# Optimization experiments

Hardware: AMD Instinct MI355X
Metric: run time of the kernel (lower is better)

Reference implementation:

```python
import jax, jax.numpy as jnp
import numpy as np

B, S, D = 2, 2048, 1024
H, DK, DV = 16, 64, 64
EPS = 1e-5
SQRT_DK = float(np.sqrt(DK))


def setup_inputs() -> dict:
    key = jax.random.key(0)
    ks = jax.random.split(key, 8)
    sc = 0.02
    return {
        "x": jax.random.normal(ks[0], (B, S, D), jnp.float32),
        "Wk": jax.random.normal(ks[1], (D, H * DK), jnp.float32) * sc,
        "bk": jnp.zeros((H * DK,), jnp.float32),
        "Wq": jax.random.normal(ks[2], (D, H * DK), jnp.float32) * sc,
        "bq": jnp.zeros((H * DK,), jnp.float32),
        "Wv": jax.random.normal(ks[3], (D, H * DV), jnp.float32) * sc,
        "bv": jnp.zeros((H * DV,), jnp.float32),
        "Wo": jax.random.normal(ks[4], (H * DV, D), jnp.float32) * sc,
        "bo": jnp.zeros((D,), jnp.float32),
        "gamma": jnp.ones((D,), jnp.float32),
        "beta": jnp.zeros((D,), jnp.float32),
    }


def reference(x, Wk, bk, Wq, bq, Wv, bv, Wo, bo, gamma, beta):
    b, s, d = x.shape
    # NOTE: original torch code reshapes (B, S, H*dk) directly to (B, H, S, dk)
    # without a transpose; we replicate that exact (non-standard) reshape.
    keys = (x @ Wk + bk).reshape(b, H, s, DK)
    queries = (x @ Wq + bq).reshape(b, H, s, DK)
    values = (x @ Wv + bv).reshape(b, H, s, DV)

    scores = jnp.einsum('bhqd,bhkd->bhqk', queries, keys) / SQRT_DK
    causal_mask = jnp.triu(jnp.ones((s, s), bool), k=1)  # True = masked
    scores = jnp.where(causal_mask[None, None], jnp.float32(-1e9), scores)
    attention = jax.nn.softmax(scores, axis=-1)

    context = jnp.einsum('bhqk,bhkd->bhqd', attention, values)
    context = context.reshape(b, s, H * DV)

    out = context @ Wo + bo  # dropout is identity at inference
    out = out + x            # residual connection

    mean = jnp.mean(out, axis=-1, keepdims=True)
    var = jnp.mean(jnp.square(out - mean), axis=-1, keepdims=True)
    return (out - mean) / jnp.sqrt(var + EPS) * gamma + beta
```

## Files before the change

### kernel.cpp

```cpp
#include <hip/hip_runtime.h>


typedef __attribute__((ext_vector_type(8))) __bf16 bf16x8;
typedef __attribute__((ext_vector_type(8))) unsigned short ushort8;
typedef __attribute__((ext_vector_type(4))) unsigned short u16x4;
typedef __attribute__((ext_vector_type(4))) float f32x4;

static __device__ __forceinline__ unsigned short f2bf(float f) {
    unsigned u = __builtin_bit_cast(unsigned, f);
    u += 0x7fffu + ((u >> 16) & 1u);
    return (unsigned short)(u >> 16);
}

static __device__ __forceinline__ float bf2f(unsigned short u) {
    return __builtin_bit_cast(float, (unsigned)u << 16);
}

__global__ __launch_bounds__(256) void prep_kernel(
    const float* __restrict__ x,
    const float* __restrict__ Wq, const float* __restrict__ Wk,
    const float* __restrict__ Wv, const float* __restrict__ Wo,
    unsigned short* __restrict__ xb, unsigned short* __restrict__ WT)
{
    const int tid = threadIdx.x;
    const int z = blockIdx.z;
    if (z == 4) {
        const int bid = blockIdx.y * 16 + blockIdx.x;
        const int base = bid * 4096 + tid;
        #pragma unroll
        for (int it = 0; it < 16; it++) {
            int i = base + it * 256;
            float4 v = ((const float4*)x)[i];
            ushort4 o;
            o.x = f2bf(v.x); o.y = f2bf(v.y); o.z = f2bf(v.z); o.w = f2bf(v.w);
            ((ushort4*)xb)[i] = o;
        }
        return;
    }
    const float* src = (z == 0) ? Wq : (z == 1) ? Wk : (z == 2) ? Wv : Wo;
    unsigned short* dst = WT + ((size_t)z << 20);
    __shared__ __align__(16) unsigned short t[64 * 68];
    const int n0 = blockIdx.x * 64, k0 = blockIdx.y * 64;
    #pragma unroll
    for (int u = 0; u < 4; u++) {
        int e = u * 256 + tid;
        int r = e >> 4, c4 = (e & 15) * 4;
        float4 v = *(const float4*)(src + (k0 + r) * 1024 + n0 + c4);
        ushort4 o;
        o.x = f2bf(v.x); o.y = f2bf(v.y); o.z = f2bf(v.z); o.w = f2bf(v.w);
        *(ushort4*)(t + r * 68 + c4) = o;
    }
    __syncthreads();
    #pragma unroll
    for (int u = 0; u < 4; u++) {
        int e = u * 256 + tid;
        int rn = e >> 4, ck = (e & 15) * 4;
        ushort4 o;
        o.x = t[(ck + 0) * 68 + rn];
        o.y = t[(ck + 1) * 68 + rn];
        o.z = t[(ck + 2) * 68 + rn];
        o.w = t[(ck + 3) * 68 + rn];
        *(ushort4*)(dst + (n0 + rn) * 1024 + k0 + ck) = o;
    }
}

__global__ __launch_bounds__(256) void vtrans_kernel(const unsigned short* __restrict__ V,
                                                     unsigned short* __restrict__ VT) {
    __shared__ __align__(16) unsigned short t[64 * 68];
    const int tid = threadIdx.x;
    const int p0 = blockIdx.x * 64;
    const long base = (long)blockIdx.y * 131072;
    #pragma unroll
    for (int u = 0; u < 2; u++) {
        int e = u * 256 + tid;
        int r = e >> 3, c8 = (e & 7) * 8;
        ushort8 v = *(const ushort8*)(V + base + (long)(p0 + r) * 64 + c8);
        *(ushort8*)(t + r * 68 + c8) = v;
    }
    __syncthreads();
    #pragma unroll
    for (int u = 0; u < 4; u++) {
        int e = u * 256 + tid;
        int dv = e >> 4, pk = (e & 15) * 4;
        ushort4 o;
        o.x = t[(pk + 0) * 68 + dv];
        o.y = t[(pk + 1) * 68 + dv];
        o.z = t[(pk + 2) * 68 + dv];
        o.w = t[(pk + 3) * 68 + dv];
        *(ushort4*)(VT + base + (long)dv * 2048 + p0 + pk) = o;
    }
}

__global__ __launch_bounds__(256, 3) void gemm_kernel(
    const unsigned short* __restrict__ A,
    const unsigned short* __restrict__ Bt,
    const float* __restrict__ b0, const float* __restrict__ b1, const float* __restrict__ b2,
    unsigned short* __restrict__ outQ, unsigned short* __restrict__ outK,
    unsigned short* __restrict__ outV,
    const float* __restrict__ resid, int mode)
{
    __shared__ __align__(16) unsigned short As[2][128 * 32];
    __shared__ __align__(16) unsigned short Bs[2][128 * 32];
    const int tid = threadIdx.x;
    const int lane = tid & 63, wave = tid >> 6;
    const int quad = lane >> 4, l16 = lane & 15;
    const int wm = wave >> 1, wn = wave & 1;
    const int row0 = blockIdx.y * 128, n0g = blockIdx.x * 128;

    const int sr = tid >> 2;
    const int sc = (tid & 3) * 8;
    const unsigned short* Ag0 = A + (size_t)(row0 + sr) * 1024 + sc;
    const unsigned short* Ag1 = A + (size_t)(row0 + 64 + sr) * 1024 + sc;
    const unsigned short* Bg0 = Bt + (size_t)(n0g + sr) * 1024 + sc;
    const unsigned short* Bg1 = Bt + (size_t)(n0g + 64 + sr) * 1024 + sc;

    {
        ushort8 a0 = *(const ushort8*)(Ag0);
        ushort8 a1 = *(const ushort8*)(Ag1);
        ushort8 bv0 = *(const ushort8*)(Bg0);
        ushort8 bv1 = *(const ushort8*)(Bg1);
        *(ushort8*)(As[0] + sr * 32 + sc) = a0;
        *(ushort8*)(As[0] + (64 + sr) * 32 + sc) = a1;
        *(ushort8*)(Bs[0] + sr * 32 + sc) = bv0;
        *(ushort8*)(Bs[0] + (64 + sr) * 32 + sc) = bv1;
    }
    __syncthreads();

    f32x4 acc[4][4] = {};
    #pragma unroll 2
    for (int it = 0; it < 32; ++it) {
        const int cur = it & 1;
        ushort8 na0, na1, nb0, nb1;
        if (it < 31) {
            const int k0 = (it + 1) * 32;
            na0 = *(const ushort8*)(Ag0 + k0);
            na1 = *(const ushort8*)(Ag1 + k0);
            nb0 = *(const ushort8*)(Bg0 + k0);
            nb1 = *(const ushort8*)(Bg1 + k0);
        }
        bf16x8 af[4], bfr[4];
        #pragma unroll
        for (int i = 0; i < 4; i++)
            af[i] = *(const bf16x8*)(As[cur] + (wm * 64 + i * 16 + l16) * 32 + quad * 8);
        #pragma unroll
        for (int j = 0; j < 4; j++)
            bfr[j] = *(const bf16x8*)(Bs[cur] + (wn * 64 + j * 16 + l16) * 32 + quad * 8);
        #pragma unroll
        for (int i = 0; i < 4; i++)
            #pragma unroll
            for (int j = 0; j < 4; j++)
                acc[i][j] = __builtin_amdgcn_mfma_f32_16x16x32_bf16(af[i], bfr[j], acc[i][j], 0, 0, 0);
        if (it < 31) {
            const int nxt = cur ^ 1;
            *(ushort8*)(As[nxt] + sr * 32 + sc) = na0;
            *(ushort8*)(As[nxt] + (64 + sr) * 32 + sc) = na1;
            *(ushort8*)(Bs[nxt] + sr * 32 + sc) = nb0;
            *(ushort8*)(Bs[nxt] + (64 + sr) * 32 + sc) = nb1;
            __syncthreads();
        }
    }

    if (mode == 0) {
        const int which = n0g >> 10;
        const float* bp = (which == 0) ? b0 : (which == 1) ? b1 : b2;
        unsigned short* op = (which == 0) ? outQ : (which == 1) ? outK : outV;
        const float scl = (which == 0) ? 0.125f : 1.0f;
        #pragma unroll
        for (int i = 0; i < 4; i++)
            #pragma unroll
            for (int j = 0; j < 4; j++) {
                int c = (n0g + wn * 64 + j * 16 + l16) & 1023;
                float bj = bp[c];
                #pragma unroll
                for (int r = 0; r < 4; r++) {
                    int r_g = row0 + wm * 64 + i * 16 + quad * 4 + r;
                    op[(size_t)r_g * 1024 + c] = f2bf((acc[i][j][r] + bj) * scl);
                }
            }
    } else {
        #pragma unroll
        for (int i = 0; i < 4; i++)
            #pragma unroll
            for (int j = 0; j < 4; j++) {
                int c_g = n0g + wn * 64 + j * 16 + l16;
                float bj = b0[c_g];
                #pragma unroll
                for (int r = 0; r < 4; r++) {
                    int r_g = row0 + wm * 64 + i * 16 + quad * 4 + r;
                    size_t idx = (size_t)r_g * 1024 + c_g;
                    outQ[idx] = f2bf(acc[i][j][r] + bj + resid[idx]);
                }
            }
    }
}

__global__ __launch_bounds__(256, 3) void flash_kernel(
    const unsigned short* __restrict__ Q,
    const unsigned short* __restrict__ K,
    const unsigned short* __restrict__ VT,
    unsigned short* __restrict__ Ctx)
{
    __shared__ __align__(16) unsigned short Kt[128 * 72];
    __shared__ __align__(16) unsigned short Vt[64 * 136];
    __shared__ __align__(16) unsigned short Pt[4][16 * 136];
    const int tid = threadIdx.x;
    const int lane = tid & 63, wave = tid >> 6;
    const int quad = lane >> 4, l16 = lane & 15;
    const int qb = 31 - blockIdx.y;
    const int q0 = qb * 64;
    const long base = (long)blockIdx.x * 131072;

    bf16x8 qa[2];
    #pragma unroll
    for (int kk = 0; kk < 2; kk++)
        qa[kk] = *(const bf16x8*)(Q + base + (q0 + wave * 16 + l16) * 64 + kk * 32 + quad * 8);

    f32x4 o[4] = {};
    float l_one = 0.f;
    const int nt = (qb + 2) >> 1;
    const int qpos = q0 + wave * 16 + l16;

    #pragma unroll
    for (int u = 0; u < 4; u++) {
        int e = u * 256 + tid;
        int r = e >> 3, c = (e & 7) * 8;
        *(ushort8*)(Kt + r * 72 + c) = *(const ushort8*)(K + base + (long)r * 64 + c);
        int dv = e >> 4, kc = (e & 15) * 8;
        *(ushort8*)(Vt + dv * 136 + kc) = *(const ushort8*)(VT + base + (long)dv * 2048 + kc);
    }
    __syncthreads();

    for (int t = 0; t < nt; t++) {
        ushort8 nk[4], nv[4];
        if (t + 1 < nt) {
            const int k1 = (t + 1) * 128;
            #pragma unroll
            for (int u = 0; u < 4; u++) {
                int e = u * 256 + tid;
                int r = e >> 3, c = (e & 7) * 8;
                nk[u] = *(const ushort8*)(K + base + (long)(k1 + r) * 64 + c);
                int dv = e >> 4, kc = (e & 15) * 8;
                nv[u] = *(const ushort8*)(VT + base + (long)dv * 2048 + k1 + kc);
            }
        }
        const int k0 = t * 128;
        const int climit = (q0 + 63 - k0) >> 4;
        const bool diag = (t == nt - 1);
        unsigned short* pw = Pt[wave];

        #pragma unroll
        for (int c = 0; c < 8; c++) {
            u16x4 pk4 = {};
            if (c <= climit) {
                bf16x8 kb0 = *(const bf16x8*)(Kt + (c * 16 + l16) * 72 + quad * 8);
                bf16x8 kb1 = *(const bf16x8*)(Kt + (c * 16 + l16) * 72 + 32 + quad * 8);
                f32x4 a = {};
                a = __builtin_amdgcn_mfma_f32_16x16x32_bf16(kb0, qa[0], a, 0, 0, 0);
                a = __builtin_amdgcn_mfma_f32_16x16x32_bf16(kb1, qa[1], a, 0, 0, 0);
                #pragma unroll
                for (int r = 0; r < 4; r++) {
                    float p = __expf(a[r]);
                    if (diag) {
                        int kpos = k0 + c * 16 + quad * 4 + r;
                        p = (kpos > qpos) ? 0.f : p;
                    }
                    a[r] = p;
                }
                l_one += (a[0] + a[1]) + (a[2] + a[3]);
                pk4[0] = f2bf(a[0]); pk4[1] = f2bf(a[1]);
                pk4[2] = f2bf(a[2]); pk4[3] = f2bf(a[3]);
            }
            *(u16x4*)(pw + l16 * 136 + c * 16 + quad * 4) = pk4;
        }

        const int kkmax = (climit >> 1) < 3 ? (climit >> 1) : 3;
        #pragma unroll
        for (int kk = 0; kk < 4; kk++) {
            if (kk <= kkmax) {
                bf16x8 pa = *(const bf16x8*)(pw + l16 * 136 + kk * 32 + quad * 8);
                #pragma unroll
                for (int c2 = 0; c2 < 4; c2++) {
                    bf16x8 vb = *(const bf16x8*)(Vt + (c2 * 16 + l16) * 136 + kk * 32 + quad * 8);
                    o[c2] = __builtin_amdgcn_mfma_f32_16x16x32_bf16(pa, vb, o[c2], 0, 0, 0);
                }
            }
        }
        __syncthreads();
        if (t + 1 < nt) {
            #pragma unroll
            for (int u = 0; u < 4; u++) {
                int e = u * 256 + tid;
                int r = e >> 3, c = (e & 7) * 8;
                *(ushort8*)(Kt + r * 72 + c) = nk[u];
                int dv = e >> 4, kc = (e & 15) * 8;
                *(ushort8*)(Vt + dv * 136 + kc) = nv[u];
            }
            __syncthreads();
        }
    }

    l_one += __shfl_xor(l_one, 16, 64);
    l_one += __shfl_xor(l_one, 32, 64);
    float rinv[4];
    #pragma unroll
    for (int r = 0; r < 4; r++)
        rinv[r] = 1.0f / __shfl(l_one, quad * 4 + r, 16);
    #pragma unroll
    for (int c2 = 0; c2 < 4; c2++)
        #pragma unroll
        for (int r = 0; r < 4; r++) {
            int row = q0 + wave * 16 + quad * 4 + r;
            Ctx[base + (long)row * 64 + c2 * 16 + l16] = f2bf(o[c2][r] * rinv[r]);
        }
}

__global__ __launch_bounds__(256) void ln_kernel(const unsigned short* __restrict__ inp,
                                                 const float* __restrict__ gamma,
                                                 const float* __restrict__ beta,
                                                 float* __restrict__ out)
{
    __shared__ float ssum[4], ssq[4];
    const int row = blockIdx.x;
    const int tid = threadIdx.x;
    ushort4 uv = ((const ushort4*)(inp + (size_t)row * 1024))[tid];
    float vx = bf2f(uv.x), vy = bf2f(uv.y), vz = bf2f(uv.z), vw = bf2f(uv.w);
    float s = vx + vy + vz + vw;
    float q = vx * vx + vy * vy + vz * vz + vw * vw;
    #pragma unroll
    for (int off = 32; off >= 1; off >>= 1) {
        s += __shfl_xor(s, off, 64);
        q += __shfl_xor(q, off, 64);
    }
    if ((tid & 63) == 0) { ssum[tid >> 6] = s; ssq[tid >> 6] = q; }
    __syncthreads();
    float ts = ssum[0] + ssum[1] + ssum[2] + ssum[3];
    float tq = ssq[0] + ssq[1] + ssq[2] + ssq[3];
    float mean = ts * (1.f / 1024.f);
    float var = tq * (1.f / 1024.f) - mean * mean;
    float rinv = rsqrtf(var + 1e-5f);
    float4 g = ((const float4*)gamma)[tid];
    float4 b = ((const float4*)beta)[tid];
    float4 o;
    o.x = (vx - mean) * rinv * g.x + b.x;
    o.y = (vy - mean) * rinv * g.y + b.y;
    o.z = (vz - mean) * rinv * g.z + b.z;
    o.w = (vw - mean) * rinv * g.w + b.w;
    ((float4*)(out + (size_t)row * 1024))[tid] = o;
}

extern "C" void kernel_launch(void* const* d_in, const int* in_sizes, int n_in,
                              void* d_out, int out_size, void* d_ws, size_t ws_size,
                              hipStream_t stream) {
    const float* x     = (const float*)d_in[0];
    const float* Wk    = (const float*)d_in[1];
    const float* bk    = (const float*)d_in[2];
    const float* Wq    = (const float*)d_in[3];
    const float* bq    = (const float*)d_in[4];
    const float* Wv    = (const float*)d_in[5];
    const float* bv    = (const float*)d_in[6];
    const float* Wo    = (const float*)d_in[7];
    const float* bo    = (const float*)d_in[8];
    const float* gamma = (const float*)d_in[9];
    const float* beta  = (const float*)d_in[10];
    float* out = (float*)d_out;

    char* ws = (char*)d_ws;
    unsigned short* xb    = (unsigned short*)(ws);
    unsigned short* WqkvT = (unsigned short*)(ws + (8ull << 20));
    unsigned short* Qb    = (unsigned short*)(ws + (16ull << 20));
    unsigned short* Kb    = (unsigned short*)(ws + (24ull << 20));
    unsigned short* VbT   = (unsigned short*)(ws + (32ull << 20));
    unsigned short* Cb    = (unsigned short*)(ws + (40ull << 20));
    unsigned short* outp  = (unsigned short*)(ws + (48ull << 20));
    unsigned short* WoT   = WqkvT + (3u << 20);
    unsigned short* Vbn   = Cb;

    dim3 pgrid(16, 16, 5);
    prep_kernel<<<pgrid, 256, 0, stream>>>(x, Wq, Wk, Wv, Wo, xb, WqkvT);

    dim3 qkvgrid(24, 32);
    gemm_kernel<<<qkvgrid, 256, 0, stream>>>(xb, WqkvT, bq, bk, bv,
                                             Qb, Kb, Vbn, nullptr, 0);

    dim3 vgrid(32, 32);
    vtrans_kernel<<<vgrid, 256, 0, stream>>>(Vbn, VbT);

    dim3 fgrid(32, 32);
    flash_kernel<<<fgrid, 256, 0, stream>>>(Qb, Kb, VbT, Cb);

    dim3 ogrid(8, 32);
    gemm_kernel<<<ogrid, 256, 0, stream>>>(Cb, WoT, bo, nullptr, nullptr,
                                           outp, nullptr, nullptr, x, 1);

    ln_kernel<<<4096, 256, 0, stream>>>(outp, gamma, beta, out);
}
```

Measured before the change: 200.4 us.

## Double flash query tile per wave and keep P in registers via permlane swaps

The flash attention kernel now processes 128 query rows per block (32 per wave, as two 16-row sub-tiles), which halves the grid and reuses each K/V tile loaded into shared memory across twice as many queries. The P probabilities no longer go through a shared-memory scratch buffer. They are converted with packed bf16 conversion instructions and rearranged into the MFMA A-operand layout using v_permlane32/16_swap, removing LDS writes and reads. Causal skipping is now per wave on the diagonal tile. The trade-offs are fewer blocks (less parallelism, a coarser causal imbalance) and higher register pressure under the existing 3-blocks-per-CU launch bound.

```diff
diff --git a/kernel.cpp b/kernel.cpp
--- a/kernel.cpp
+++ b/kernel.cpp
@@ -5,6 +5,7 @@
 typedef __attribute__((ext_vector_type(8))) unsigned short ushort8;
 typedef __attribute__((ext_vector_type(4))) unsigned short u16x4;
 typedef __attribute__((ext_vector_type(4))) float f32x4;
+typedef __attribute__((ext_vector_type(4))) unsigned int u32x4;
 
 static __device__ __forceinline__ unsigned short f2bf(float f) {
     unsigned u = __builtin_bit_cast(unsigned, f);
@@ -14,6 +15,12 @@
 
 static __device__ __forceinline__ float bf2f(unsigned short u) {
     return __builtin_bit_cast(float, (unsigned)u << 16);
+}
+
+static __device__ __forceinline__ unsigned cvt_pk_bf16(float lo, float hi) {
+    unsigned r;
+    asm("v_cvt_pk_bf16_f32 %0, %1, %2" : "=v"(r) : "v"(lo), "v"(hi));
+    return r;
 }
 
 __global__ __launch_bounds__(256) void prep_kernel(
@@ -202,23 +209,24 @@
 {
     __shared__ __align__(16) unsigned short Kt[128 * 72];
     __shared__ __align__(16) unsigned short Vt[64 * 136];
-    __shared__ __align__(16) unsigned short Pt[4][16 * 136];
     const int tid = threadIdx.x;
     const int lane = tid & 63, wave = tid >> 6;
     const int quad = lane >> 4, l16 = lane & 15;
-    const int qb = 31 - blockIdx.y;
-    const int q0 = qb * 64;
+    const int qb = 15 - blockIdx.y;
+    const int q0 = qb * 128;
     const long base = (long)blockIdx.x * 131072;
-
-    bf16x8 qa[2];
-    #pragma unroll
-    for (int kk = 0; kk < 2; kk++)
-        qa[kk] = *(const bf16x8*)(Q + base + (q0 + wave * 16 + l16) * 64 + kk * 32 + quad * 8);
-
-    f32x4 o[4] = {};
-    float l_one = 0.f;
-    const int nt = (qb + 2) >> 1;
-    const int qpos = q0 + wave * 16 + l16;
+    const int nt = qb + 1;
+
+    bf16x8 qa[2][2];
+    #pragma unroll
+    for (int s = 0; s < 2; s++)
+        #pragma unroll
+        for (int h = 0; h < 2; h++)
+            qa[s][h] = *(const bf16x8*)(Q + base + (q0 + wave * 32 + s * 16 + l16) * 64 + h * 32 + quad * 8);
+
+    f32x4 o[2][4] = {};
+    float l_one[2] = {0.f, 0.f};
+    const int qpos0 = q0 + wave * 32 + l16;
 
     #pragma unroll
     for (int u = 0; u < 4; u++) {
@@ -244,44 +252,72 @@
             }
         }
         const int k0 = t * 128;
-        const int climit = (q0 + 63 - k0) >> 4;
         const bool diag = (t == nt - 1);
-        unsigned short* pw = Pt[wave];
-
-        #pragma unroll
-        for (int c = 0; c < 8; c++) {
-            u16x4 pk4 = {};
-            if (c <= climit) {
-                bf16x8 kb0 = *(const bf16x8*)(Kt + (c * 16 + l16) * 72 + quad * 8);
-                bf16x8 kb1 = *(const bf16x8*)(Kt + (c * 16 + l16) * 72 + 32 + quad * 8);
-                f32x4 a = {};
-                a = __builtin_amdgcn_mfma_f32_16x16x32_bf16(kb0, qa[0], a, 0, 0, 0);
-                a = __builtin_amdgcn_mfma_f32_16x16x32_bf16(kb1, qa[1], a, 0, 0, 0);
-                #pragma unroll
-                for (int r = 0; r < 4; r++) {
-                    float p = __expf(a[r]);
-                    if (diag) {
-                        int kpos = k0 + c * 16 + quad * 4 + r;
-                        p = (kpos > qpos) ? 0.f : p;
-                    }
-                    a[r] = p;
-                }
-                l_one += (a[0] + a[1]) + (a[2] + a[3]);
-                pk4[0] = f2bf(a[0]); pk4[1] = f2bf(a[1]);
-                pk4[2] = f2bf(a[2]); pk4[3] = f2bf(a[3]);
-            }
-            *(u16x4*)(pw + l16 * 136 + c * 16 + quad * 4) = pk4;
-        }
-
-        const int kkmax = (climit >> 1) < 3 ? (climit >> 1) : 3;
+        const int kkmax = diag ? wave : 3;
+
         #pragma unroll
         for (int kk = 0; kk < 4; kk++) {
             if (kk <= kkmax) {
-                bf16x8 pa = *(const bf16x8*)(pw + l16 * 136 + kk * 32 + quad * 8);
+                const int cE = kk * 2, cO = kk * 2 + 1;
+                f32x4 aE[2], aO[2];
+                {
+                    bf16x8 kb0 = *(const bf16x8*)(Kt + (cE * 16 + l16) * 72 + quad * 8);
+                    bf16x8 kb1 = *(const bf16x8*)(Kt + (cE * 16 + l16) * 72 + 32 + quad * 8);
+                    #pragma unroll
+                    for (int s = 0; s < 2; s++) {
+                        f32x4 z = {};
+                        z = __builtin_amdgcn_mfma_f32_16x16x32_bf16(kb0, qa[s][0], z, 0, 0, 0);
+                        z = __builtin_amdgcn_mfma_f32_16x16x32_bf16(kb1, qa[s][1], z, 0, 0, 0);
+                        aE[s] = z;
+                    }
+                }
+                {
+                    bf16x8 kb0 = *(const bf16x8*)(Kt + (cO * 16 + l16) * 72 + quad * 8);
+                    bf16x8 kb1 = *(const bf16x8*)(Kt + (cO * 16 + l16) * 72 + 32 + quad * 8);
+                    #pragma unroll
+                    for (int s = 0; s < 2; s++) {
+                        f32x4 z = {};
+                        z = __builtin_amdgcn_mfma_f32_16x16x32_bf16(kb0, qa[s][0], z, 0, 0, 0);
+                        z = __builtin_amdgcn_mfma_f32_16x16x32_bf16(kb1, qa[s][1], z, 0, 0, 0);
+                        aO[s] = z;
+                    }
+                }
+                bf16x8 pa[2];
+                #pragma unroll
+                for (int s = 0; s < 2; s++) {
+                    float pE[4], pO[4];
+                    #pragma unroll
+                    for (int r = 0; r < 4; r++) {
+                        float e1 = __expf(aE[s][r]);
+                        float e2 = __expf(aO[s][r]);
+                        if (diag) {
+                            int kE = k0 + cE * 16 + quad * 4 + r;
+                            int kO = k0 + cO * 16 + quad * 4 + r;
+                            int qp = qpos0 + s * 16;
+                            e1 = (kE > qp) ? 0.f : e1;
+                            e2 = (kO > qp) ? 0.f : e2;
+                        }
+                        pE[r] = e1; pO[r] = e2;
+                    }
+                    l_one[s] += (pE[0] + pE[1]) + (pE[2] + pE[3])
+                              + (pO[0] + pO[1]) + (pO[2] + pO[3]);
+                    unsigned w0 = cvt_pk_bf16(pE[0], pE[1]);
+                    unsigned w1 = cvt_pk_bf16(pE[2], pE[3]);
+                    unsigned w2 = cvt_pk_bf16(pO[0], pO[1]);
+                    unsigned w3 = cvt_pk_bf16(pO[2], pO[3]);
+                    asm("v_permlane32_swap_b32 %0, %1" : "+v"(w0), "+v"(w2));
+                    asm("v_permlane16_swap_b32 %0, %1" : "+v"(w0), "+v"(w2));
+                    asm("v_permlane32_swap_b32 %0, %1" : "+v"(w1), "+v"(w3));
+                    asm("v_permlane16_swap_b32 %0, %1" : "+v"(w1), "+v"(w3));
+                    u32x4 pu;
+                    pu[0] = w0; pu[1] = w1; pu[2] = w2; pu[3] = w3;
+                    pa[s] = __builtin_bit_cast(bf16x8, pu);
+                }
                 #pragma unroll
                 for (int c2 = 0; c2 < 4; c2++) {
                     bf16x8 vb = *(const bf16x8*)(Vt + (c2 * 16 + l16) * 136 + kk * 32 + quad * 8);
-                    o[c2] = __builtin_amdgcn_mfma_f32_16x16x32_bf16(pa, vb, o[c2], 0, 0, 0);
+                    o[0][c2] = __builtin_amdgcn_mfma_f32_16x16x32_bf16(pa[0], vb, o[0][c2], 0, 0, 0);
+                    o[1][c2] = __builtin_amdgcn_mfma_f32_16x16x32_bf16(pa[1], vb, o[1][c2], 0, 0, 0);
                 }
             }
         }
@@ -299,19 +335,23 @@
         }
     }
 
-    l_one += __shfl_xor(l_one, 16, 64);
-    l_one += __shfl_xor(l_one, 32, 64);
-    float rinv[4];
-    #pragma unroll
-    for (int r = 0; r < 4; r++)
-        rinv[r] = 1.0f / __shfl(l_one, quad * 4 + r, 16);
-    #pragma unroll
-    for (int c2 = 0; c2 < 4; c2++)
-        #pragma unroll
-        for (int r = 0; r < 4; r++) {
-            int row = q0 + wave * 16 + quad * 4 + r;
-            Ctx[base + (long)row * 64 + c2 * 16 + l16] = f2bf(o[c2][r] * rinv[r]);
-        }
+    #pragma unroll
+    for (int s = 0; s < 2; s++) {
+        float l = l_one[s];
+        l += __shfl_xor(l, 16, 64);
+        l += __shfl_xor(l, 32, 64);
+        float rinv[4];
+        #pragma unroll
+        for (int r = 0; r < 4; r++)
+            rinv[r] = 1.0f / __shfl(l, quad * 4 + r, 16);
+        #pragma unroll
+        for (int c2 = 0; c2 < 4; c2++)
+            #pragma unroll
+            for (int r = 0; r < 4; r++) {
+                int row = q0 + wave * 32 + s * 16 + quad * 4 + r;
+                Ctx[base + (long)row * 64 + c2 * 16 + l16] = f2bf(o[s][c2][r] * rinv[r]);
+            }
+    }
 }
 
 __global__ __launch_bounds__(256) void ln_kernel(const unsigned short* __restrict__ inp,
@@ -385,7 +425,7 @@
     dim3 vgrid(32, 32);
     vtrans_kernel<<<vgrid, 256, 0, stream>>>(Vbn, VbT);
 
-    dim3 fgrid(32, 32);
+    dim3 fgrid(32, 16);
     flash_kernel<<<fgrid, 256, 0, stream>>>(Qb, Kb, VbT, Cb);
 
     dim3 ogrid(8, 32);
```

Result: slower. 231.9 us (+15.8%).

## Keep softmax probabilities in registers via permlane swaps instead of LDS round-trip

Applied to the files above, without the earlier changes.

Removes the per-wave shared-memory P buffer. Scores for two 16-key chunks are computed together, exponentiated, packed to bf16 with v_cvt_pk_bf16_f32, and rearranged across lanes with permlane32/permlane16 swaps so they feed the PV MFMA directly as the A operand. Diagonal-tile work is now bounded per wave rather than per block. Freeing the LDS allows raising the occupancy hint from 3 to 4 blocks, at the cost of possible register pressure and a dependence on the lane-permutation mapping being exactly right.

```diff
diff --git a/kernel.cpp b/kernel.cpp
--- a/kernel.cpp
+++ b/kernel.cpp
@@ -5,6 +5,7 @@
 typedef __attribute__((ext_vector_type(8))) unsigned short ushort8;
 typedef __attribute__((ext_vector_type(4))) unsigned short u16x4;
 typedef __attribute__((ext_vector_type(4))) float f32x4;
+typedef __attribute__((ext_vector_type(4))) unsigned int u32x4;
 
 static __device__ __forceinline__ unsigned short f2bf(float f) {
     unsigned u = __builtin_bit_cast(unsigned, f);
@@ -14,6 +15,12 @@
 
 static __device__ __forceinline__ float bf2f(unsigned short u) {
     return __builtin_bit_cast(float, (unsigned)u << 16);
+}
+
+static __device__ __forceinline__ unsigned cvt_pk_bf16(float lo, float hi) {
+    unsigned r;
+    asm("v_cvt_pk_bf16_f32 %0, %1, %2" : "=v"(r) : "v"(lo), "v"(hi));
+    return r;
 }
 
 __global__ __launch_bounds__(256) void prep_kernel(
@@ -194,7 +201,7 @@
     }
 }
 
-__global__ __launch_bounds__(256, 3) void flash_kernel(
+__global__ __launch_bounds__(256, 4) void flash_kernel(
     const unsigned short* __restrict__ Q,
     const unsigned short* __restrict__ K,
     const unsigned short* __restrict__ VT,
@@ -202,22 +209,21 @@
 {
     __shared__ __align__(16) unsigned short Kt[128 * 72];
     __shared__ __align__(16) unsigned short Vt[64 * 136];
-    __shared__ __align__(16) unsigned short Pt[4][16 * 136];
     const int tid = threadIdx.x;
     const int lane = tid & 63, wave = tid >> 6;
     const int quad = lane >> 4, l16 = lane & 15;
     const int qb = 31 - blockIdx.y;
     const int q0 = qb * 64;
     const long base = (long)blockIdx.x * 131072;
+    const int nt = (qb + 2) >> 1;
 
     bf16x8 qa[2];
     #pragma unroll
-    for (int kk = 0; kk < 2; kk++)
-        qa[kk] = *(const bf16x8*)(Q + base + (q0 + wave * 16 + l16) * 64 + kk * 32 + quad * 8);
+    for (int h = 0; h < 2; h++)
+        qa[h] = *(const bf16x8*)(Q + base + (q0 + wave * 16 + l16) * 64 + h * 32 + quad * 8);
 
     f32x4 o[4] = {};
     float l_one = 0.f;
-    const int nt = (qb + 2) >> 1;
     const int qpos = q0 + wave * 16 + l16;
 
     #pragma unroll
@@ -244,40 +250,52 @@
             }
         }
         const int k0 = t * 128;
-        const int climit = (q0 + 63 - k0) >> 4;
         const bool diag = (t == nt - 1);
-        unsigned short* pw = Pt[wave];
-
-        #pragma unroll
-        for (int c = 0; c < 8; c++) {
-            u16x4 pk4 = {};
-            if (c <= climit) {
-                bf16x8 kb0 = *(const bf16x8*)(Kt + (c * 16 + l16) * 72 + quad * 8);
-                bf16x8 kb1 = *(const bf16x8*)(Kt + (c * 16 + l16) * 72 + 32 + quad * 8);
-                f32x4 a = {};
-                a = __builtin_amdgcn_mfma_f32_16x16x32_bf16(kb0, qa[0], a, 0, 0, 0);
-                a = __builtin_amdgcn_mfma_f32_16x16x32_bf16(kb1, qa[1], a, 0, 0, 0);
+        const int kkmax = diag ? ((q0 - k0 + wave * 16 + 15) >> 5) : 3;
+
+        #pragma unroll
+        for (int kk = 0; kk < 4; kk++) {
+            if (kk <= kkmax) {
+                const int cE = kk * 2, cO = kk * 2 + 1;
+                f32x4 aE = {}, aO = {};
+                {
+                    bf16x8 kb0 = *(const bf16x8*)(Kt + (cE * 16 + l16) * 72 + quad * 8);
+                    bf16x8 kb1 = *(const bf16x8*)(Kt + (cE * 16 + l16) * 72 + 32 + quad * 8);
+                    aE = __builtin_amdgcn_mfma_f32_16x16x32_bf16(kb0, qa[0], aE, 0, 0, 0);
+                    aE = __builtin_amdgcn_mfma_f32_16x16x32_bf16(kb1, qa[1], aE, 0, 0, 0);
+                }
+                {
+                    bf16x8 kb0 = *(const bf16x8*)(Kt + (cO * 16 + l16) * 72 + quad * 8);
+                    bf16x8 kb1 = *(const bf16x8*)(Kt + (cO * 16 + l16) * 72 + 32 + quad * 8);
+                    aO = __builtin_amdgcn_mfma_f32_16x16x32_bf16(kb0, qa[0], aO, 0, 0, 0);
+                    aO = __builtin_amdgcn_mfma_f32_16x16x32_bf16(kb1, qa[1], aO, 0, 0, 0);
+                }
+                float pE[4], pO[4];
                 #pragma unroll
                 for (int r = 0; r < 4; r++) {
-                    float p = __expf(a[r]);
+                    float e1 = __expf(aE[r]);
+                    float e2 = __expf(aO[r]);
                     if (diag) {
-                        int kpos = k0 + c * 16 + quad * 4 + r;
-                        p = (kpos > qpos) ? 0.f : p;
+                        int kE = k0 + cE * 16 + quad * 4 + r;
+                        int kO = k0 + cO * 16 + quad * 4 + r;
+                        e1 = (kE > qpos) ? 0.f : e1;
+                        e2 = (kO > qpos) ? 0.f : e2;
                     }
-                    a[r] = p;
-                }
-                l_one += (a[0] + a[1]) + (a[2] + a[3]);
-                pk4[0] = f2bf(a[0]); pk4[1] = f2bf(a[1]);
-                pk4[2] = f2bf(a[2]); pk4[3] = f2bf(a[3]);
-            }
-            *(u16x4*)(pw + l16 * 136 + c * 16 + quad * 4) = pk4;
-        }
-
-        const int kkmax = (climit >> 1) < 3 ? (climit >> 1) : 3;
-        #pragma unroll
-        for (int kk = 0; kk < 4; kk++) {
-            if (kk <= kkmax) {
-                bf16x8 pa = *(const bf16x8*)(pw + l16 * 136 + kk * 32 + quad * 8);
+                    pE[r] = e1; pO[r] = e2;
+                }
+                l_one += (pE[0] + pE[1]) + (pE[2] + pE[3])
+                       + (pO[0] + pO[1]) + (pO[2] + pO[3]);
+                unsigned w0 = cvt_pk_bf16(pE[0], pE[1]);
+                unsigned w1 = cvt_pk_bf16(pE[2], pE[3]);
+                unsigned w2 = cvt_pk_bf16(pO[0], pO[1]);
+                unsigned w3 = cvt_pk_bf16(pO[2], pO[3]);
+                asm("v_permlane32_swap_b32 %0, %1" : "+v"(w0), "+v"(w2));
+                asm("v_permlane16_swap_b32 %0, %1" : "+v"(w0), "+v"(w2));
+                asm("v_permlane32_swap_b32 %0, %1" : "+v"(w1), "+v"(w3));
+                asm("v_permlane16_swap_b32 %0, %1" : "+v"(w1), "+v"(w3));
+                u32x4 pu;
+                pu[0] = w0; pu[1] = w1; pu[2] = w2; pu[3] = w3;
+                bf16x8 pa = __builtin_bit_cast(bf16x8, pu);
                 #pragma unroll
                 for (int c2 = 0; c2 < 4; c2++) {
                     bf16x8 vb = *(const bf16x8*)(Vt + (c2 * 16 + l16) * 136 + kk * 32 + quad * 8);
```

Measured after the change: 202.7 us. Within noise of the previous version (+1.2%).
